# Performance work log

Hardware: AMD Instinct MI355X
Metric: run time of the kernel (lower is better)

Reference implementation:

```python
import jax, jax.numpy as jnp
import numpy as np

B, S, A = 65536, 376, 17
H1, H2, K = 400, 300, 15
MAX_ACTION = 1.0


def setup_inputs() -> dict:
    key = jax.random.key(0)
    ks = jax.random.split(key, 16)

    def lin(kw, fan_in, fan_out):
        lim = 1.0 / np.sqrt(fan_in)
        k1, k2 = jax.random.split(kw)
        W = jax.random.uniform(k1, (fan_in, fan_out), jnp.float32, -lim, lim)
        b = jax.random.uniform(k2, (fan_out,), jnp.float32, -lim, lim)
        return W, b

    W1, b1 = lin(ks[0], S, H1)
    W2, b2 = lin(ks[1], H1, H2)
    Wmu, bmu = lin(ks[2], H2, A)
    Wlv, blv = lin(ks[3], H2, A)
    Wu, bu = lin(ks[4], H2, K * A)
    Ww, bw = lin(ks[5], H2, K * A)
    Wb, bb = lin(ks[6], H2, K)
    x = jax.random.normal(ks[7], (B, S), jnp.float32)
    eps = jax.random.normal(ks[8], (B, A), jnp.float32)
    return dict(x=x, eps=eps, W1=W1, b1=b1, W2=W2, b2=b2, Wmu=Wmu, bmu=bmu,
                Wlv=Wlv, blv=blv, Wu=Wu, bu=bu, Ww=Ww, bw=bw, Wb=Wb, bb=bb)


def _flow_chain(action, u, w, b):
    # u, w: (K, B, A); b: (K, B). Sequential planar flow -> lax.scan over K.
    def step(carry, uwb):
        z, ldj = carry
        u_k, w_k, b_k = uwb
        uw = jnp.sum(w_k * u_k, -1)                       # (B,)
        m_uw = -1.0 + jax.nn.softplus(uw)
        w_norm_sq = jnp.sum(w_k * w_k, -1)
        u_hat = u_k + ((m_uw - uw) / w_norm_sq)[:, None] * w_k  # invertibility reparam
        wzb = jnp.sum(w_k * z, -1) + b_k                  # (B,)
        t = jnp.tanh(wzb)
        z_new = z + u_hat * t[:, None]
        psi_u = jnp.sum(w_k * u_hat, -1) * (1.0 - t * t)  # psi^T u_hat
        ldj_new = ldj + jnp.log(jnp.abs(1.0 + psi_u))
        return (z_new, ldj_new), None

    init = (action, jnp.zeros(action.shape[0], action.dtype))
    (z_fin, ldj), _ = jax.lax.scan(step, init, (u, w, b))
    return z_fin, ldj


def reference(x, eps, W1, b1, W2, b2, Wmu, bmu, Wlv, blv, Wu, bu, Ww, bw, Wb, bb):
    h = jax.nn.relu(x @ W1 + b1)
    h = jax.nn.relu(h @ W2 + b2)
    mu = MAX_ACTION * jnp.tanh(h @ Wmu + bmu)
    log_var = MAX_ACTION * jnp.tanh(h @ Wlv + blv)
    std = jnp.exp(log_var)                 # torch code uses log_var.exp() as the scale
    action = mu + std * eps                # rsample

    u = (h @ Wu + bu).reshape(B, K, A).transpose(1, 0, 2)   # (K, B, A)
    w = (h @ Ww + bw).reshape(B, K, A).transpose(1, 0, 2)   # (K, B, A)
    b = (h @ Wb + bb).T                                      # (K, B)

    final_action, log_det_j = _flow_chain(action, u, w, b)

    # Normal(mu, std).log_prob(action) summed over action dim; (action-mu)/std == eps
    log_2pi = jnp.float32(np.log(2.0 * np.pi))
    log_prob = jnp.sum(-0.5 * eps * eps - log_var - 0.5 * log_2pi, axis=-1)
    log_prob_final = log_prob - log_det_j
    prob_final = jnp.exp(log_prob_final)
    return final_action, prob_final, log_prob_final
```

## Files before the change

kernel.cpp:

```cpp
#include <hip/hip_runtime.h>

typedef unsigned short ushort_t;
typedef unsigned int uint_t;
typedef __bf16 bf16x8 __attribute__((ext_vector_type(8)));
typedef float f32x4 __attribute__((ext_vector_type(4)));

#define B_ROWS 65536

#define KT1 12
#define NT1 30
#define KTC1 15
#define KI2 13
#define NT2 20
#define KTC2 10
#define KI3 10
#define NT3 50
#define LDH3 25


#define SZ1 (NT1 * KT1 * 512)
#define SZ2 (NT2 * KI2 * 512)
#define SZ3 (NT3 * KI3 * 512)

__device__ inline float bf2f(ushort_t u) {
    union { uint_t i; float f; } x; x.i = ((uint_t)u) << 16; return x.f;
}
__device__ inline ushort_t f2bf(float f) {
    uint_t u = __float_as_uint(f);
    return (ushort_t)((u + 0x7FFFu + ((u >> 16) & 1u)) >> 16);
}
__device__ inline uint_t pack2(float a, float b) {
    return (uint_t)f2bf(a) | ((uint_t)f2bf(b) << 16);
}
__device__ inline float fast_tanh(float x) {
    float e = __expf(2.f * x);
    return 1.f - 2.f / (e + 1.f);
}
__device__ inline void gl2lds16(const ushort_t* g, ushort_t* l) {
    __builtin_amdgcn_global_load_lds(
        (const __attribute__((address_space(1))) uint_t*)g,
        (__attribute__((address_space(3))) uint_t*)l, 16, 0, 0);
}

__global__ void pack_kernel(const float* __restrict__ W1, const float* __restrict__ W2,
                            const float* __restrict__ Wmu, const float* __restrict__ Wlv,
                            const float* __restrict__ Wu, const float* __restrict__ Ww,
                            const float* __restrict__ Wb,
                            const float* __restrict__ b1, const float* __restrict__ b2,
                            const float* __restrict__ bmu, const float* __restrict__ blv,
                            const float* __restrict__ bu, const float* __restrict__ bw,
                            const float* __restrict__ bb,
                            ushort_t* __restrict__ W1t, ushort_t* __restrict__ W2t,
                            ushort_t* __restrict__ Wht,
                            float* __restrict__ b1p, float* __restrict__ b2p,
                            float* __restrict__ bHp)
{
    int i = blockIdx.x * 256 + threadIdx.x;
    if (i < SZ1) {
        int t = i >> 9, pos = i & 511;
        int l = pos >> 3, j = pos & 7;
        int n = (t / KT1) * 16 + (l & 15);
        int k = (t % KT1) * 32 + (l >> 4) * 8 + j;
        W1t[i] = (n < 400 && k < 376) ? f2bf(W1[k * 400 + n]) : (ushort_t)0;
    } else if (i < SZ1 + SZ2) {
        int i2 = i - SZ1;
        int t = i2 >> 9, pos = i2 & 511;
        int l = pos >> 3, j = pos & 7;
        int n = (t / KI2) * 16 + (l & 15);
        int k = (t % KI2) * 32 + (l >> 4) * 8 + j;
        W2t[i2] = (n < 300 && k < 400) ? f2bf(W2[k * 300 + n]) : (ushort_t)0;
    } else if (i < SZ1 + SZ2 + SZ3) {
        int i3 = i - SZ1 - SZ2;
        int t = i3 >> 9, pos = i3 & 511;
        int l = pos >> 3, j = pos & 7;
        int n = (t / KI3) * 16 + (l & 15);
        int k = (t % KI3) * 32 + (l >> 4) * 8 + j;
        float v = 0.f;
        if (k < 300) {
            if (n < 24)      { if (n < 17) v = Wmu[k * 17 + n]; }
            else if (n < 48) { int c = n - 24; if (c < 17) v = Wlv[k * 17 + c]; }
            else if (n < 64) { int c = n - 48; if (c < 15) v = Wb[k * 15 + c]; }
            else if (n < 784) {
                int r = n - 64, slot = r / 48, c = r % 48;
                if (c < 24) { if (c < 17) v = Wu[k * 255 + slot * 17 + c]; }
                else        { int c2 = c - 24; if (c2 < 17) v = Ww[k * 255 + slot * 17 + c2]; }
            }
        }
        Wht[i3] = f2bf(v);
    } else {
        int j = i - SZ1 - SZ2 - SZ3;
        if (j < 480) {
            b1p[j] = (j < 400) ? b1[j] : 0.f;
        } else if (j < 800) {
            int n = j - 480;
            b2p[n] = (n < 300) ? b2[n] : 0.f;
        } else if (j < 1600) {
            int n = j - 800;
            float v = 0.f;
            if (n < 24)      { if (n < 17) v = bmu[n]; }
            else if (n < 48) { int c = n - 24; if (c < 17) v = blv[c]; }
            else if (n < 64) { int c = n - 48; if (c < 15) v = bb[c]; }
            else if (n < 784) {
                int r = n - 64, slot = r / 48, c = r % 48;
                if (c < 24) { if (c < 17) v = bu[slot * 17 + c]; }
                else        { int c2 = c - 24; if (c2 < 17) v = bw[slot * 17 + c2]; }
            }
            bHp[n] = v;
        }
    }
}

__global__ __launch_bounds__(256)
void cvt_kernel(const float* __restrict__ x, ushort_t* __restrict__ xt, int nUnits)
{
    int U = blockIdx.x * 256 + threadIdx.x;
    if (U >= nUnits) return;
    int t = U >> 6, l = U & 63;
    int rowblk = t / KT1, kblk = t - rowblk * KT1;
    long row = (long)rowblk * 16 + (l & 15);
    int k0 = kblk * 32 + (l >> 4) * 8;
    uint4 o = {0u, 0u, 0u, 0u};
    if (k0 + 8 <= 376) {
        const float4* p = reinterpret_cast<const float4*>(x + row * 376 + k0);
        float4 v0 = p[0], v1 = p[1];
        o.x = pack2(v0.x, v0.y); o.y = pack2(v0.z, v0.w);
        o.z = pack2(v1.x, v1.y); o.w = pack2(v1.z, v1.w);
    }
    reinterpret_cast<uint4*>(xt)[U] = o;
}

template<bool RELU, bool OUT_TILED>
__global__ __launch_bounds__(256)
void gemm_tile(const ushort_t* __restrict__ A, const ushort_t* __restrict__ Bt,
               const float* __restrict__ bias, ushort_t* __restrict__ C,
               int kTA, int kIters, int kTC)
{
    __shared__ ushort_t As[8 * 512];
    __shared__ ushort_t Bs[10 * 512];
    const int tid = threadIdx.x;
    const int lane = tid & 63, wv = tid >> 6;
    const int q = lane >> 4, l16 = lane & 15;
    const int nb0 = blockIdx.x * 10;
    const int rowblk0 = blockIdx.y * 8;

    f32x4 acc[2][10];
    #pragma unroll
    for (int r = 0; r < 2; ++r)
        #pragma unroll
        for (int c = 0; c < 10; ++c)
            acc[r][c] = (f32x4){0.f, 0.f, 0.f, 0.f};

    for (int kt = 0; kt < kIters; ++kt) {
        #pragma unroll
        for (int i = 0; i < 2; ++i) {
            int t = wv * 2 + i;
            gl2lds16(A + (((size_t)(rowblk0 + t) * kTA + kt) << 9) + lane * 8,
                     &As[t << 9]);
        }
        #pragma unroll
        for (int t2 = 0; t2 < 3; ++t2) {
            int t = wv + t2 * 4;
            if (t < 10)
                gl2lds16(Bt + (((size_t)(nb0 + t) * kIters + kt) << 9) + lane * 8,
                         &Bs[t << 9]);
        }
        __syncthreads();

        bf16x8 a0 = __builtin_bit_cast(bf16x8,
            *reinterpret_cast<const uint4*>(&As[((wv * 2 + 0) << 9) + lane * 8]));
        bf16x8 a1 = __builtin_bit_cast(bf16x8,
            *reinterpret_cast<const uint4*>(&As[((wv * 2 + 1) << 9) + lane * 8]));
        #pragma unroll
        for (int c = 0; c < 10; ++c) {
            bf16x8 b = __builtin_bit_cast(bf16x8,
                *reinterpret_cast<const uint4*>(&Bs[(c << 9) + lane * 8]));
            acc[0][c] = __builtin_amdgcn_mfma_f32_16x16x32_bf16(a0, b, acc[0][c], 0, 0, 0);
            acc[1][c] = __builtin_amdgcn_mfma_f32_16x16x32_bf16(a1, b, acc[1][c], 0, 0, 0);
        }
        __syncthreads();
    }

    #pragma unroll
    for (int r = 0; r < 2; ++r) {
        int rowblk = rowblk0 + wv * 2 + r;
        #pragma unroll
        for (int c = 0; c < 10; ++c) {
            int n = (nb0 + c) * 16 + l16;
            float bv = bias[n];
            #pragma unroll
            for (int reg = 0; reg < 4; ++reg) {
                float v = acc[r][c][reg] + bv;
                if (RELU) v = fmaxf(v, 0.f);
                int mrow = q * 4 + reg;
                if (OUT_TILED) {
                    size_t off = (((size_t)rowblk * kTC + (n >> 5)) << 9)
                               + (size_t)(((n >> 3) & 3) * 16 + mrow) * 8 + (n & 7);
                    C[off] = f2bf(v);
                } else {
                    long m = (long)rowblk * 16 + mrow;
                    C[m * (long)kTC + n] = f2bf(v);
                }
            }
        }
    }
}

__device__ inline void ld_group8(const ushort_t* hb, int g, float* dst) {
    uint4 v = *reinterpret_cast<const uint4*>(hb + ((g >> 2) << 9) + ((g & 3) << 7));
    uint_t q[4] = {v.x, v.y, v.z, v.w};
    #pragma unroll
    for (int m = 0; m < 4; ++m) {
        dst[2 * m]     = __uint_as_float(q[m] << 16);
        dst[2 * m + 1] = __uint_as_float(q[m] & 0xFFFF0000u);
    }
}

__global__ __launch_bounds__(256, 4)
void flow_kernel(const ushort_t* __restrict__ heads, const float* __restrict__ eps,
                 float* __restrict__ out, int rowBase, int Btot)
{
    const int tid = threadIdx.x;
    const int sub = tid & 3;
    const long row = (long)blockIdx.x * 64 + (tid >> 2);
    const ushort_t* hb = heads + (((size_t)(row >> 4) * LDH3) << 9)
                               + (size_t)((row & 15) << 3);

    float z[8];
    float lp = 0.f;
    {
        float amu[8] = {0,0,0,0,0,0,0,0}, alv[8] = {0,0,0,0,0,0,0,0};
        if (sub < 3) {
            ld_group8(hb, sub, amu);
            ld_group8(hb, 3 + sub, alv);
        }
        float ep[8];
        #pragma unroll
        for (int c = 0; c < 8; ++c) {
            int i = sub * 8 + c;
            ep[c] = (i < 17) ? eps[row * 17 + i] : 0.f;
        }
        #pragma unroll
        for (int c = 0; c < 8; ++c) {
            float mu = fast_tanh(amu[c]);
            float lv = fast_tanh(alv[c]);
            z[c] = mu + __expf(lv) * ep[c];
            int i = sub * 8 + c;
            lp += (i < 17) ? (-0.5f * ep[c] * ep[c] - lv - 0.918938533f) : 0.f;
        }
    }

    float bv[16];
    ld_group8(hb, 6, &bv[0]);
    ld_group8(hb, 7, &bv[8]);

    float ldj = 0.f;
    #pragma unroll
    for (int k = 0; k < 15; ++k) {
        float au[8] = {0,0,0,0,0,0,0,0}, aw[8] = {0,0,0,0,0,0,0,0};
        if (sub < 3) {
            ld_group8(hb, 8 + 6 * k + sub, au);
            ld_group8(hb, 11 + 6 * k + sub, aw);
        }
        float uw = 0.f, w2 = 0.f, wz = 0.f;
        #pragma unroll
        for (int c = 0; c < 8; ++c) {
            uw += aw[c] * au[c];
            w2 += aw[c] * aw[c];
            wz += aw[c] * z[c];
        }
        uw += __shfl_xor(uw, 1); uw += __shfl_xor(uw, 2);
        w2 += __shfl_xor(w2, 1); w2 += __shfl_xor(w2, 2);
        wz += __shfl_xor(wz, 1); wz += __shfl_xor(wz, 2);

        float sp = (uw > 15.f) ? uw : __logf(1.f + __expf(uw));
        float m = sp - 1.f;
        float coef = (m - uw) / fmaxf(w2, 1e-20f);
        float t = fast_tanh(wz + bv[k]);
        #pragma unroll
        for (int c = 0; c < 8; ++c)
            z[c] += (au[c] + coef * aw[c]) * t;
        float psi = m * (1.f - t * t);
        ldj += __logf(fmaxf(fabsf(1.f + psi), 1e-30f));
    }

    lp += __shfl_xor(lp, 1); lp += __shfl_xor(lp, 2);
    const long g = rowBase + row;
    #pragma unroll
    for (int c = 0; c < 8; ++c) {
        int i = sub * 8 + c;
        if (i < 17) out[g * 17 + i] = z[c];
    }
    float lpf = lp - ldj;
    if (sub == 0) {
        out[(long)Btot * 17 + g] = __expf(lpf);
        out[(long)Btot * 18 + g] = lpf;
    }
}

extern "C" void kernel_launch(void* const* d_in, const int* in_sizes, int n_in,
                              void* d_out, int out_size, void* d_ws, size_t ws_size,
                              hipStream_t stream)
{
    const float* x   = (const float*)d_in[0];
    const float* eps = (const float*)d_in[1];
    float* out = (float*)d_out;

    const size_t wUS = (size_t)SZ1 + SZ2 + SZ3;
    const size_t fixedBytes = wUS * 2 + (480 + 320 + 800) * 4;
    int Mc = 2048;
    {
        const int cand[6] = {65536, 32768, 16384, 8192, 4096, 2048};
        for (int i = 0; i < 6; ++i) {
            size_t req = (size_t)cand[i] * 2368 + fixedBytes;
            if (req <= ws_size) { Mc = cand[i]; break; }
        }
    }

    ushort_t* region1 = (ushort_t*)d_ws;
    ushort_t* region2 = region1 + (size_t)Mc * 800;
    ushort_t* W1t = region2 + (size_t)Mc * 384;
    ushort_t* W2t = W1t + SZ1;
    ushort_t* Wht = W2t + SZ2;
    float* b1p = (float*)(Wht + SZ3);
    float* b2p = b1p + 480;
    float* bHp = b2p + 320;

    const int packN = SZ1 + SZ2 + SZ3 + 1600;
    pack_kernel<<<(packN + 255) / 256, 256, 0, stream>>>(
        (const float*)d_in[2],  (const float*)d_in[4],
        (const float*)d_in[6],  (const float*)d_in[8],
        (const float*)d_in[10], (const float*)d_in[12], (const float*)d_in[14],
        (const float*)d_in[3],  (const float*)d_in[5],
        (const float*)d_in[7],  (const float*)d_in[9],
        (const float*)d_in[11], (const float*)d_in[13], (const float*)d_in[15],
        W1t, W2t, Wht, b1p, b2p, bHp);

    const int nChunks = B_ROWS / Mc;
    const int nUnits = Mc * 48;
    for (int c = 0; c < nChunks; ++c) {
        const float* xc = x + (size_t)c * Mc * 376;
        cvt_kernel<<<(nUnits + 255) / 256, 256, 0, stream>>>(xc, region2, nUnits);
        gemm_tile<true, true><<<dim3(3, Mc / 128), 256, 0, stream>>>(
            region2, W1t, b1p, region1, KT1, KT1, KTC1);
        gemm_tile<true, true><<<dim3(2, Mc / 128), 256, 0, stream>>>(
            region1, W2t, b2p, region2, KTC1, KI2, KTC2);
        gemm_tile<false, true><<<dim3(5, Mc / 128), 256, 0, stream>>>(
            region2, Wht, bHp, region1, KTC2, KI3, LDH3);
        flow_kernel<<<Mc / 64, 256, 0, stream>>>(region1, eps + (size_t)c * Mc * 17,
                                                 out, c * Mc, B_ROWS);
    }
}
```

Baseline: 366.5 us.

## Fuse conversion, three GEMMs and flow chain into one LDS-resident kernel

Replaces the chunked pipeline of convert, three tiled GEMM launches and the flow kernel with a single fused kernel. Each 64-row block converts x to bf16 in LDS, runs all three GEMM layers with activations kept in shared memory, then computes the planar flow from LDS. Weights are read straight from global memory (L2) instead of being staged in LDS. This removes the global round-trips of the intermediate activations and the extra launches, at the cost of about 150 KB of LDS per block, which limits occupancy, and weight reloads in every block.

```diff
diff --git a/kernel.cpp b/kernel.cpp
--- a/kernel.cpp
+++ b/kernel.cpp
@@ -15,16 +15,19 @@
 #define KTC2 10
 #define KI3 10
 #define NT3 50
-#define LDH3 25
+#define KTH 25
 
 
 #define SZ1 (NT1 * KT1 * 512)
 #define SZ2 (NT2 * KI2 * 512)
 #define SZ3 (NT3 * KI3 * 512)
 
-__device__ inline float bf2f(ushort_t u) {
-    union { uint_t i; float f; } x; x.i = ((uint_t)u) << 16; return x.f;
-}
+#define P_X  0
+#define P_H1 24576
+#define P_H2 55296
+#define P_HD 0
+#define SM_TOT 75776
+
 __device__ inline ushort_t f2bf(float f) {
     uint_t u = __float_as_uint(f);
     return (ushort_t)((u + 0x7FFFu + ((u >> 16) & 1u)) >> 16);
@@ -36,10 +39,13 @@
     float e = __expf(2.f * x);
     return 1.f - 2.f / (e + 1.f);
 }
-__device__ inline void gl2lds16(const ushort_t* g, ushort_t* l) {
-    __builtin_amdgcn_global_load_lds(
-        (const __attribute__((address_space(1))) uint_t*)g,
-        (__attribute__((address_space(3))) uint_t*)l, 16, 0, 0);
+__device__ inline void unpack8(uint4 v, float* dst) {
+    uint_t q[4] = {v.x, v.y, v.z, v.w};
+    #pragma unroll
+    for (int m = 0; m < 4; ++m) {
+        dst[2 * m]     = __uint_as_float(q[m] << 16);
+        dst[2 * m + 1] = __uint_as_float(q[m] & 0xFFFF0000u);
+    }
 }
 
 __global__ void pack_kernel(const float* __restrict__ W1, const float* __restrict__ W2,
@@ -110,190 +116,185 @@
     }
 }
 
-__global__ __launch_bounds__(256)
-void cvt_kernel(const float* __restrict__ x, ushort_t* __restrict__ xt, int nUnits)
+template<int KITERS, bool RELU>
+__device__ __forceinline__ void phase_gemm(
+    ushort_t* sm, int aBase, int ktA,
+    const ushort_t* __restrict__ Bt, const float* __restrict__ bias,
+    int cBase, int ktC, int NT, int lane, int wv)
 {
-    int U = blockIdx.x * 256 + threadIdx.x;
-    if (U >= nUnits) return;
-    int t = U >> 6, l = U & 63;
-    int rowblk = t / KT1, kblk = t - rowblk * KT1;
-    long row = (long)rowblk * 16 + (l & 15);
-    int k0 = kblk * 32 + (l >> 4) * 8;
-    uint4 o = {0u, 0u, 0u, 0u};
-    if (k0 + 8 <= 376) {
-        const float4* p = reinterpret_cast<const float4*>(x + row * 376 + k0);
-        float4 v0 = p[0], v1 = p[1];
-        o.x = pack2(v0.x, v0.y); o.y = pack2(v0.z, v0.w);
-        o.z = pack2(v1.x, v1.y); o.w = pack2(v1.z, v1.w);
-    }
-    reinterpret_cast<uint4*>(xt)[U] = o;
-}
-
-template<bool RELU, bool OUT_TILED>
-__global__ __launch_bounds__(256)
-void gemm_tile(const ushort_t* __restrict__ A, const ushort_t* __restrict__ Bt,
-               const float* __restrict__ bias, ushort_t* __restrict__ C,
-               int kTA, int kIters, int kTC)
+    const int n0 = (NT * wv) >> 3;
+    const int cnt = ((NT * (wv + 1)) >> 3) - n0;
+
+    f32x4 acc[4][7];
+    #pragma unroll
+    for (int rt = 0; rt < 4; ++rt)
+        #pragma unroll
+        for (int c = 0; c < 7; ++c)
+            acc[rt][c] = (f32x4){0.f, 0.f, 0.f, 0.f};
+
+    #pragma unroll
+    for (int kt = 0; kt < KITERS; ++kt) {
+        bf16x8 a[4];
+        #pragma unroll
+        for (int rt = 0; rt < 4; ++rt)
+            a[rt] = __builtin_bit_cast(bf16x8, *reinterpret_cast<const uint4*>(
+                &sm[aBase + ((rt * ktA + kt) << 9) + lane * 8]));
+        #pragma unroll
+        for (int c = 0; c < 7; ++c) {
+            if (c < cnt) {
+                bf16x8 b = __builtin_bit_cast(bf16x8, *reinterpret_cast<const uint4*>(
+                    Bt + (((size_t)(n0 + c) * KITERS + kt) << 9) + lane * 8));
+                #pragma unroll
+                for (int rt = 0; rt < 4; ++rt)
+                    acc[rt][c] = __builtin_amdgcn_mfma_f32_16x16x32_bf16(
+                        a[rt], b, acc[rt][c], 0, 0, 0);
+            }
+        }
+    }
+
+    const int q = lane >> 4, l16 = lane & 15;
+    #pragma unroll
+    for (int c = 0; c < 7; ++c) {
+        if (c < cnt) {
+            int n = (n0 + c) * 16 + l16;
+            float bv = bias[n];
+            #pragma unroll
+            for (int rt = 0; rt < 4; ++rt) {
+                #pragma unroll
+                for (int reg = 0; reg < 4; ++reg) {
+                    float v = acc[rt][c][reg] + bv;
+                    if (RELU) v = fmaxf(v, 0.f);
+                    int r16 = q * 4 + reg;
+                    sm[cBase + ((rt * ktC + (n >> 5)) << 9) + (((n >> 3) & 3) << 7)
+                       + (r16 << 3) + (n & 7)] = f2bf(v);
+                }
+            }
+        }
+    }
+}
+
+__global__ __launch_bounds__(512, 2)
+void fused_kernel(const float* __restrict__ x, const float* __restrict__ eps,
+                  const ushort_t* __restrict__ W1t, const ushort_t* __restrict__ W2t,
+                  const ushort_t* __restrict__ Wht,
+                  const float* __restrict__ b1p, const float* __restrict__ b2p,
+                  const float* __restrict__ bHp,
+                  float* __restrict__ out)
 {
-    __shared__ ushort_t As[8 * 512];
-    __shared__ ushort_t Bs[10 * 512];
+    __shared__ ushort_t sm[SM_TOT];
     const int tid = threadIdx.x;
     const int lane = tid & 63, wv = tid >> 6;
-    const int q = lane >> 4, l16 = lane & 15;
-    const int nb0 = blockIdx.x * 10;
-    const int rowblk0 = blockIdx.y * 8;
-
-    f32x4 acc[2][10];
-    #pragma unroll
-    for (int r = 0; r < 2; ++r)
-        #pragma unroll
-        for (int c = 0; c < 10; ++c)
-            acc[r][c] = (f32x4){0.f, 0.f, 0.f, 0.f};
-
-    for (int kt = 0; kt < kIters; ++kt) {
-        #pragma unroll
-        for (int i = 0; i < 2; ++i) {
-            int t = wv * 2 + i;
-            gl2lds16(A + (((size_t)(rowblk0 + t) * kTA + kt) << 9) + lane * 8,
-                     &As[t << 9]);
-        }
-        #pragma unroll
-        for (int t2 = 0; t2 < 3; ++t2) {
-            int t = wv + t2 * 4;
-            if (t < 10)
-                gl2lds16(Bt + (((size_t)(nb0 + t) * kIters + kt) << 9) + lane * 8,
-                         &Bs[t << 9]);
-        }
-        __syncthreads();
-
-        bf16x8 a0 = __builtin_bit_cast(bf16x8,
-            *reinterpret_cast<const uint4*>(&As[((wv * 2 + 0) << 9) + lane * 8]));
-        bf16x8 a1 = __builtin_bit_cast(bf16x8,
-            *reinterpret_cast<const uint4*>(&As[((wv * 2 + 1) << 9) + lane * 8]));
-        #pragma unroll
-        for (int c = 0; c < 10; ++c) {
-            bf16x8 b = __builtin_bit_cast(bf16x8,
-                *reinterpret_cast<const uint4*>(&Bs[(c << 9) + lane * 8]));
-            acc[0][c] = __builtin_amdgcn_mfma_f32_16x16x32_bf16(a0, b, acc[0][c], 0, 0, 0);
-            acc[1][c] = __builtin_amdgcn_mfma_f32_16x16x32_bf16(a1, b, acc[1][c], 0, 0, 0);
-        }
-        __syncthreads();
-    }
-
-    #pragma unroll
-    for (int r = 0; r < 2; ++r) {
-        int rowblk = rowblk0 + wv * 2 + r;
-        #pragma unroll
-        for (int c = 0; c < 10; ++c) {
-            int n = (nb0 + c) * 16 + l16;
-            float bv = bias[n];
-            #pragma unroll
-            for (int reg = 0; reg < 4; ++reg) {
-                float v = acc[r][c][reg] + bv;
-                if (RELU) v = fmaxf(v, 0.f);
-                int mrow = q * 4 + reg;
-                if (OUT_TILED) {
-                    size_t off = (((size_t)rowblk * kTC + (n >> 5)) << 9)
-                               + (size_t)(((n >> 3) & 3) * 16 + mrow) * 8 + (n & 7);
-                    C[off] = f2bf(v);
-                } else {
-                    long m = (long)rowblk * 16 + mrow;
-                    C[m * (long)kTC + n] = f2bf(v);
-                }
-            }
-        }
-    }
-}
-
-__device__ inline void ld_group8(const ushort_t* hb, int g, float* dst) {
-    uint4 v = *reinterpret_cast<const uint4*>(hb + ((g >> 2) << 9) + ((g & 3) << 7));
-    uint_t q[4] = {v.x, v.y, v.z, v.w};
-    #pragma unroll
-    for (int m = 0; m < 4; ++m) {
-        dst[2 * m]     = __uint_as_float(q[m] << 16);
-        dst[2 * m + 1] = __uint_as_float(q[m] & 0xFFFF0000u);
-    }
-}
-
-__global__ __launch_bounds__(256, 4)
-void flow_kernel(const ushort_t* __restrict__ heads, const float* __restrict__ eps,
-                 float* __restrict__ out, int rowBase, int Btot)
-{
-    const int tid = threadIdx.x;
-    const int sub = tid & 3;
-    const long row = (long)blockIdx.x * 64 + (tid >> 2);
-    const ushort_t* hb = heads + (((size_t)(row >> 4) * LDH3) << 9)
-                               + (size_t)((row & 15) << 3);
-
-    float z[8];
-    float lp = 0.f;
-    {
-        float amu[8] = {0,0,0,0,0,0,0,0}, alv[8] = {0,0,0,0,0,0,0,0};
-        if (sub < 3) {
-            ld_group8(hb, sub, amu);
-            ld_group8(hb, 3 + sub, alv);
-        }
-        float ep[8];
+    const long row0 = (long)blockIdx.x * 64;
+
+    #pragma unroll
+    for (int it = 0; it < 6; ++it) {
+        int u = it * 512 + tid;
+        int row = u / 48, ku = u - row * 48;
+        uint4 o = {0u, 0u, 0u, 0u};
+        if (ku < 47) {
+            const float4* p = reinterpret_cast<const float4*>(
+                x + (row0 + row) * 376 + ku * 8);
+            float4 v0 = p[0], v1 = p[1];
+            o.x = pack2(v0.x, v0.y); o.y = pack2(v0.z, v0.w);
+            o.z = pack2(v1.x, v1.y); o.w = pack2(v1.z, v1.w);
+        }
+        *reinterpret_cast<uint4*>(
+            &sm[P_X + (((row >> 4) * KT1 + (ku >> 2)) << 9) + ((ku & 3) << 7)
+                + ((row & 15) << 3)]) = o;
+    }
+    __syncthreads();
+
+    phase_gemm<KT1, true>(sm, P_X, KT1, W1t, b1p, P_H1, KTC1, NT1, lane, wv);
+    __syncthreads();
+
+    phase_gemm<KI2, true>(sm, P_H1, KTC1, W2t, b2p, P_H2, KTC2, NT2, lane, wv);
+    __syncthreads();
+
+    phase_gemm<KI3, false>(sm, P_H2, KTC2, Wht, bHp, P_HD, KTH, NT3, lane, wv);
+    __syncthreads();
+
+    if (tid < 256) {
+        const int sub = tid & 3;
+        const int row = tid >> 2;
+        const int hb = P_HD + (((row >> 4) * KTH) << 9) + ((row & 15) << 3);
+        const long grow = row0 + row;
+
+        float z[8];
+        float lp = 0.f;
+        {
+            float amu[8] = {0,0,0,0,0,0,0,0}, alv[8] = {0,0,0,0,0,0,0,0};
+            if (sub < 3) {
+                unpack8(*reinterpret_cast<const uint4*>(
+                    &sm[hb + ((sub >> 2) << 9) + ((sub & 3) << 7)]), amu);
+                int g = 3 + sub;
+                unpack8(*reinterpret_cast<const uint4*>(
+                    &sm[hb + ((g >> 2) << 9) + ((g & 3) << 7)]), alv);
+            }
+            float ep[8];
+            #pragma unroll
+            for (int c = 0; c < 8; ++c) {
+                int i = sub * 8 + c;
+                ep[c] = (i < 17) ? eps[grow * 17 + i] : 0.f;
+            }
+            #pragma unroll
+            for (int c = 0; c < 8; ++c) {
+                float mu = fast_tanh(amu[c]);
+                float lv = fast_tanh(alv[c]);
+                z[c] = mu + __expf(lv) * ep[c];
+                int i = sub * 8 + c;
+                lp += (i < 17) ? (-0.5f * ep[c] * ep[c] - lv - 0.918938533f) : 0.f;
+            }
+        }
+
+        float bv[16];
+        unpack8(*reinterpret_cast<const uint4*>(&sm[hb + 512 + 256]), &bv[0]);
+        unpack8(*reinterpret_cast<const uint4*>(&sm[hb + 512 + 384]), &bv[8]);
+
+        float ldj = 0.f;
+        #pragma unroll
+        for (int k = 0; k < 15; ++k) {
+            float au[8] = {0,0,0,0,0,0,0,0}, aw[8] = {0,0,0,0,0,0,0,0};
+            if (sub < 3) {
+                int gu = 8 + 6 * k + sub;
+                int gw = 11 + 6 * k + sub;
+                unpack8(*reinterpret_cast<const uint4*>(
+                    &sm[hb + ((gu >> 2) << 9) + ((gu & 3) << 7)]), au);
+                unpack8(*reinterpret_cast<const uint4*>(
+                    &sm[hb + ((gw >> 2) << 9) + ((gw & 3) << 7)]), aw);
+            }
+            float uw = 0.f, w2 = 0.f, wz = 0.f;
+            #pragma unroll
+            for (int c = 0; c < 8; ++c) {
+                uw += aw[c] * au[c];
+                w2 += aw[c] * aw[c];
+                wz += aw[c] * z[c];
+            }
+            uw += __shfl_xor(uw, 1); uw += __shfl_xor(uw, 2);
+            w2 += __shfl_xor(w2, 1); w2 += __shfl_xor(w2, 2);
+            wz += __shfl_xor(wz, 1); wz += __shfl_xor(wz, 2);
+
+            float sp = (uw > 15.f) ? uw : __logf(1.f + __expf(uw));
+            float m = sp - 1.f;
+            float coef = (m - uw) / fmaxf(w2, 1e-20f);
+            float t = fast_tanh(wz + bv[k]);
+            #pragma unroll
+            for (int c = 0; c < 8; ++c)
+                z[c] += (au[c] + coef * aw[c]) * t;
+            float psi = m * (1.f - t * t);
+            ldj += __logf(fmaxf(fabsf(1.f + psi), 1e-30f));
+        }
+
+        lp += __shfl_xor(lp, 1); lp += __shfl_xor(lp, 2);
         #pragma unroll
         for (int c = 0; c < 8; ++c) {
             int i = sub * 8 + c;
-            ep[c] = (i < 17) ? eps[row * 17 + i] : 0.f;
-        }
-        #pragma unroll
-        for (int c = 0; c < 8; ++c) {
-            float mu = fast_tanh(amu[c]);
-            float lv = fast_tanh(alv[c]);
-            z[c] = mu + __expf(lv) * ep[c];
-            int i = sub * 8 + c;
-            lp += (i < 17) ? (-0.5f * ep[c] * ep[c] - lv - 0.918938533f) : 0.f;
-        }
-    }
-
-    float bv[16];
-    ld_group8(hb, 6, &bv[0]);
-    ld_group8(hb, 7, &bv[8]);
-
-    float ldj = 0.f;
-    #pragma unroll
-    for (int k = 0; k < 15; ++k) {
-        float au[8] = {0,0,0,0,0,0,0,0}, aw[8] = {0,0,0,0,0,0,0,0};
-        if (sub < 3) {
-            ld_group8(hb, 8 + 6 * k + sub, au);
-            ld_group8(hb, 11 + 6 * k + sub, aw);
-        }
-        float uw = 0.f, w2 = 0.f, wz = 0.f;
-        #pragma unroll
-        for (int c = 0; c < 8; ++c) {
-            uw += aw[c] * au[c];
-            w2 += aw[c] * aw[c];
-            wz += aw[c] * z[c];
-        }
-        uw += __shfl_xor(uw, 1); uw += __shfl_xor(uw, 2);
-        w2 += __shfl_xor(w2, 1); w2 += __shfl_xor(w2, 2);
-        wz += __shfl_xor(wz, 1); wz += __shfl_xor(wz, 2);
-
-        float sp = (uw > 15.f) ? uw : __logf(1.f + __expf(uw));
-        float m = sp - 1.f;
-        float coef = (m - uw) / fmaxf(w2, 1e-20f);
-        float t = fast_tanh(wz + bv[k]);
-        #pragma unroll
-        for (int c = 0; c < 8; ++c)
-            z[c] += (au[c] + coef * aw[c]) * t;
-        float psi = m * (1.f - t * t);
-        ldj += __logf(fmaxf(fabsf(1.f + psi), 1e-30f));
-    }
-
-    lp += __shfl_xor(lp, 1); lp += __shfl_xor(lp, 2);
-    const long g = rowBase + row;
-    #pragma unroll
-    for (int c = 0; c < 8; ++c) {
-        int i = sub * 8 + c;
-        if (i < 17) out[g * 17 + i] = z[c];
-    }
-    float lpf = lp - ldj;
-    if (sub == 0) {
-        out[(long)Btot * 17 + g] = __expf(lpf);
-        out[(long)Btot * 18 + g] = lpf;
+            if (i < 17) out[grow * 17 + i] = z[c];
+        }
+        float lpf = lp - ldj;
+        if (sub == 0) {
+            out[(long)B_ROWS * 17 + grow] = __expf(lpf);
+            out[(long)B_ROWS * 18 + grow] = lpf;
+        }
     }
 }
 
@@ -305,20 +306,7 @@
     const float* eps = (const float*)d_in[1];
     float* out = (float*)d_out;
 
-    const size_t wUS = (size_t)SZ1 + SZ2 + SZ3;
-    const size_t fixedBytes = wUS * 2 + (480 + 320 + 800) * 4;
-    int Mc = 2048;
-    {
-        const int cand[6] = {65536, 32768, 16384, 8192, 4096, 2048};
-        for (int i = 0; i < 6; ++i) {
-            size_t req = (size_t)cand[i] * 2368 + fixedBytes;
-            if (req <= ws_size) { Mc = cand[i]; break; }
-        }
-    }
-
-    ushort_t* region1 = (ushort_t*)d_ws;
-    ushort_t* region2 = region1 + (size_t)Mc * 800;
-    ushort_t* W1t = region2 + (size_t)Mc * 384;
+    ushort_t* W1t = (ushort_t*)d_ws;
     ushort_t* W2t = W1t + SZ1;
     ushort_t* Wht = W2t + SZ2;
     float* b1p = (float*)(Wht + SZ3);
@@ -335,18 +323,6 @@
         (const float*)d_in[11], (const float*)d_in[13], (const float*)d_in[15],
         W1t, W2t, Wht, b1p, b2p, bHp);
 
-    const int nChunks = B_ROWS / Mc;
-    const int nUnits = Mc * 48;
-    for (int c = 0; c < nChunks; ++c) {
-        const float* xc = x + (size_t)c * Mc * 376;
-        cvt_kernel<<<(nUnits + 255) / 256, 256, 0, stream>>>(xc, region2, nUnits);
-        gemm_tile<true, true><<<dim3(3, Mc / 128), 256, 0, stream>>>(
-            region2, W1t, b1p, region1, KT1, KT1, KTC1);
-        gemm_tile<true, true><<<dim3(2, Mc / 128), 256, 0, stream>>>(
-            region1, W2t, b2p, region2, KTC1, KI2, KTC2);
-        gemm_tile<false, true><<<dim3(5, Mc / 128), 256, 0, stream>>>(
-            region2, Wht, bHp, region1, KTC2, KI3, LDH3);
-        flow_kernel<<<Mc / 64, 256, 0, stream>>>(region1, eps + (size_t)c * Mc * 17,
-                                                 out, c * Mc, B_ROWS);
-    }
-}
+    fused_kernel<<<B_ROWS / 64, 512, 0, stream>>>(
+        x, eps, W1t, W2t, Wht, b1p, b2p, bHp, out);
+}
```

Measured after the change: 408.6 us. +11.5%, slower.

## Fuse fp32→bf16 conversion into first GEMM, double-buffer LDS, drop chunk loop

Applied to the files above, without the earlier changes.

The separate cvt_kernel goes away: the first GEMM now reads fp32 x directly, converts it to bf16 in registers and stages it into LDS. All GEMMs gain double-buffered LDS tiles so the next k-slice loads while MFMAs run on the current one, and use a block swizzle that groups row blocks by XCD. The per-chunk host loop is replaced by single full-batch launches with fixed workspace regions, which assumes a large enough workspace and removes the fallback sizing. LDS use per block doubles, which may lower occupancy.

```diff
diff --git a/kernel.cpp b/kernel.cpp
--- a/kernel.cpp
+++ b/kernel.cpp
@@ -15,16 +15,16 @@
 #define KTC2 10
 #define KI3 10
 #define NT3 50
-#define LDH3 25
+#define KTH 25
 
 
 #define SZ1 (NT1 * KT1 * 512)
 #define SZ2 (NT2 * KI2 * 512)
 #define SZ3 (NT3 * KI3 * 512)
 
-__device__ inline float bf2f(ushort_t u) {
-    union { uint_t i; float f; } x; x.i = ((uint_t)u) << 16; return x.f;
-}
+#define H2_US  ((size_t)4096 * KTC2 * 512)
+#define HEADS_US ((size_t)4096 * KTH * 512)
+
 __device__ inline ushort_t f2bf(float f) {
     uint_t u = __float_as_uint(f);
     return (ushort_t)((u + 0x7FFFu + ((u >> 16) & 1u)) >> 16);
@@ -40,6 +40,14 @@
     __builtin_amdgcn_global_load_lds(
         (const __attribute__((address_space(1))) uint_t*)g,
         (__attribute__((address_space(3))) uint_t*)l, 16, 0, 0);
+}
+__device__ inline void unpack8(uint4 v, float* dst) {
+    uint_t q[4] = {v.x, v.y, v.z, v.w};
+    #pragma unroll
+    for (int m = 0; m < 4; ++m) {
+        dst[2 * m]     = __uint_as_float(q[m] << 16);
+        dst[2 * m + 1] = __uint_as_float(q[m] & 0xFFFF0000u);
+    }
 }
 
 __global__ void pack_kernel(const float* __restrict__ W1, const float* __restrict__ W2,
@@ -110,38 +118,31 @@
     }
 }
 
+template<int KITERS, int NX, bool RELU, bool CVT_A>
 __global__ __launch_bounds__(256)
-void cvt_kernel(const float* __restrict__ x, ushort_t* __restrict__ xt, int nUnits)
+void gemm_db(const ushort_t* __restrict__ At, const float* __restrict__ xf,
+             const ushort_t* __restrict__ Bt, const float* __restrict__ bias,
+             ushort_t* __restrict__ C, int kTA, int kTC)
 {
-    int U = blockIdx.x * 256 + threadIdx.x;
-    if (U >= nUnits) return;
-    int t = U >> 6, l = U & 63;
-    int rowblk = t / KT1, kblk = t - rowblk * KT1;
-    long row = (long)rowblk * 16 + (l & 15);
-    int k0 = kblk * 32 + (l >> 4) * 8;
-    uint4 o = {0u, 0u, 0u, 0u};
-    if (k0 + 8 <= 376) {
-        const float4* p = reinterpret_cast<const float4*>(x + row * 376 + k0);
-        float4 v0 = p[0], v1 = p[1];
-        o.x = pack2(v0.x, v0.y); o.y = pack2(v0.z, v0.w);
-        o.z = pack2(v1.x, v1.y); o.w = pack2(v1.z, v1.w);
-    }
-    reinterpret_cast<uint4*>(xt)[U] = o;
-}
-
-template<bool RELU, bool OUT_TILED>
-__global__ __launch_bounds__(256)
-void gemm_tile(const ushort_t* __restrict__ A, const ushort_t* __restrict__ Bt,
-               const float* __restrict__ bias, ushort_t* __restrict__ C,
-               int kTA, int kIters, int kTC)
-{
-    __shared__ ushort_t As[8 * 512];
-    __shared__ ushort_t Bs[10 * 512];
+    __shared__ ushort_t As[2][8 * 512];
+    __shared__ ushort_t Bs[2][10 * 512];
     const int tid = threadIdx.x;
     const int lane = tid & 63, wv = tid >> 6;
     const int q = lane >> 4, l16 = lane & 15;
-    const int nb0 = blockIdx.x * 10;
-    const int rowblk0 = blockIdx.y * 8;
+
+    const int b = blockIdx.x;
+    const int xcd = b & 7, idx = b >> 3;
+    const int grp = idx / NX;
+    const int bx = idx - grp * NX;
+    const int by = xcd + grp * 8;
+    const int nb0 = bx * 10;
+    const int rowblk0 = by * 8;
+
+    const int ct = tid >> 6;
+    const int cl = tid & 63;
+    const int crow0 = (rowblk0 + ct) * 16 + (cl & 15);
+    const int crow1 = (rowblk0 + ct + 4) * 16 + (cl & 15);
+    const int ckoff = (cl >> 4) * 8;
 
     f32x4 acc[2][10];
     #pragma unroll
@@ -150,32 +151,91 @@
         for (int c = 0; c < 10; ++c)
             acc[r][c] = (f32x4){0.f, 0.f, 0.f, 0.f};
 
-    for (int kt = 0; kt < kIters; ++kt) {
+    if (CVT_A) {
+        #pragma unroll
+        for (int j = 0; j < 2; ++j) {
+            int row = j ? crow1 : crow0;
+            int k0 = ckoff;
+            uint4 o = {0u, 0u, 0u, 0u};
+            if (k0 + 8 <= 376) {
+                const float4* p = reinterpret_cast<const float4*>(
+                    xf + (size_t)row * 376 + k0);
+                float4 v0 = p[0], v1 = p[1];
+                o.x = pack2(v0.x, v0.y); o.y = pack2(v0.z, v0.w);
+                o.z = pack2(v1.x, v1.y); o.w = pack2(v1.z, v1.w);
+            }
+            *reinterpret_cast<uint4*>(&As[0][((ct + 4 * j) << 9) + (cl << 3)]) = o;
+        }
+    } else {
         #pragma unroll
         for (int i = 0; i < 2; ++i) {
             int t = wv * 2 + i;
-            gl2lds16(A + (((size_t)(rowblk0 + t) * kTA + kt) << 9) + lane * 8,
-                     &As[t << 9]);
-        }
-        #pragma unroll
-        for (int t2 = 0; t2 < 3; ++t2) {
-            int t = wv + t2 * 4;
-            if (t < 10)
-                gl2lds16(Bt + (((size_t)(nb0 + t) * kIters + kt) << 9) + lane * 8,
-                         &Bs[t << 9]);
-        }
-        __syncthreads();
+            gl2lds16(At + (((size_t)(rowblk0 + t) * kTA + 0) << 9) + lane * 8,
+                     &As[0][t << 9]);
+        }
+    }
+    #pragma unroll
+    for (int t2 = 0; t2 < 3; ++t2) {
+        int t = wv + t2 * 4;
+        if (t < 10)
+            gl2lds16(Bt + (((size_t)(nb0 + t) * KITERS + 0) << 9) + lane * 8,
+                     &Bs[0][t << 9]);
+    }
+    __syncthreads();
+
+    #pragma unroll
+    for (int kt = 0; kt < KITERS; ++kt) {
+        const int p = kt & 1;
+        uint4 nxt0, nxt1;
+        if (kt + 1 < KITERS) {
+            if (CVT_A) {
+                int k0 = (kt + 1) * 32 + ckoff;
+                nxt0 = (uint4){0u, 0u, 0u, 0u};
+                nxt1 = (uint4){0u, 0u, 0u, 0u};
+                if (k0 + 8 <= 376) {
+                    const float4* p0 = reinterpret_cast<const float4*>(
+                        xf + (size_t)crow0 * 376 + k0);
+                    float4 v0 = p0[0], v1 = p0[1];
+                    nxt0.x = pack2(v0.x, v0.y); nxt0.y = pack2(v0.z, v0.w);
+                    nxt0.z = pack2(v1.x, v1.y); nxt0.w = pack2(v1.z, v1.w);
+                    const float4* p1 = reinterpret_cast<const float4*>(
+                        xf + (size_t)crow1 * 376 + k0);
+                    float4 u0 = p1[0], u1 = p1[1];
+                    nxt1.x = pack2(u0.x, u0.y); nxt1.y = pack2(u0.z, u0.w);
+                    nxt1.z = pack2(u1.x, u1.y); nxt1.w = pack2(u1.z, u1.w);
+                }
+            } else {
+                #pragma unroll
+                for (int i = 0; i < 2; ++i) {
+                    int t = wv * 2 + i;
+                    gl2lds16(At + (((size_t)(rowblk0 + t) * kTA + kt + 1) << 9) + lane * 8,
+                             &As[p ^ 1][t << 9]);
+                }
+            }
+            #pragma unroll
+            for (int t2 = 0; t2 < 3; ++t2) {
+                int t = wv + t2 * 4;
+                if (t < 10)
+                    gl2lds16(Bt + (((size_t)(nb0 + t) * KITERS + kt + 1) << 9) + lane * 8,
+                             &Bs[p ^ 1][t << 9]);
+            }
+        }
 
         bf16x8 a0 = __builtin_bit_cast(bf16x8,
-            *reinterpret_cast<const uint4*>(&As[((wv * 2 + 0) << 9) + lane * 8]));
+            *reinterpret_cast<const uint4*>(&As[p][((wv * 2 + 0) << 9) + lane * 8]));
         bf16x8 a1 = __builtin_bit_cast(bf16x8,
-            *reinterpret_cast<const uint4*>(&As[((wv * 2 + 1) << 9) + lane * 8]));
+            *reinterpret_cast<const uint4*>(&As[p][((wv * 2 + 1) << 9) + lane * 8]));
         #pragma unroll
         for (int c = 0; c < 10; ++c) {
-            bf16x8 b = __builtin_bit_cast(bf16x8,
-                *reinterpret_cast<const uint4*>(&Bs[(c << 9) + lane * 8]));
-            acc[0][c] = __builtin_amdgcn_mfma_f32_16x16x32_bf16(a0, b, acc[0][c], 0, 0, 0);
-            acc[1][c] = __builtin_amdgcn_mfma_f32_16x16x32_bf16(a1, b, acc[1][c], 0, 0, 0);
+            bf16x8 bb = __builtin_bit_cast(bf16x8,
+                *reinterpret_cast<const uint4*>(&Bs[p][(c << 9) + lane * 8]));
+            acc[0][c] = __builtin_amdgcn_mfma_f32_16x16x32_bf16(a0, bb, acc[0][c], 0, 0, 0);
+            acc[1][c] = __builtin_amdgcn_mfma_f32_16x16x32_bf16(a1, bb, acc[1][c], 0, 0, 0);
+        }
+
+        if (CVT_A && kt + 1 < KITERS) {
+            *reinterpret_cast<uint4*>(&As[p ^ 1][(ct << 9) + (cl << 3)]) = nxt0;
+            *reinterpret_cast<uint4*>(&As[p ^ 1][((ct + 4) << 9) + (cl << 3)]) = nxt1;
         }
         __syncthreads();
     }
@@ -192,14 +252,9 @@
                 float v = acc[r][c][reg] + bv;
                 if (RELU) v = fmaxf(v, 0.f);
                 int mrow = q * 4 + reg;
-                if (OUT_TILED) {
-                    size_t off = (((size_t)rowblk * kTC + (n >> 5)) << 9)
-                               + (size_t)(((n >> 3) & 3) * 16 + mrow) * 8 + (n & 7);
-                    C[off] = f2bf(v);
-                } else {
-                    long m = (long)rowblk * 16 + mrow;
-                    C[m * (long)kTC + n] = f2bf(v);
-                }
+                size_t off = (((size_t)rowblk * kTC + (n >> 5)) << 9)
+                           + (size_t)(((n >> 3) & 3) * 16 + mrow) * 8 + (n & 7);
+                C[off] = f2bf(v);
             }
         }
     }
@@ -207,22 +262,17 @@
 
 __device__ inline void ld_group8(const ushort_t* hb, int g, float* dst) {
     uint4 v = *reinterpret_cast<const uint4*>(hb + ((g >> 2) << 9) + ((g & 3) << 7));
-    uint_t q[4] = {v.x, v.y, v.z, v.w};
-    #pragma unroll
-    for (int m = 0; m < 4; ++m) {
-        dst[2 * m]     = __uint_as_float(q[m] << 16);
-        dst[2 * m + 1] = __uint_as_float(q[m] & 0xFFFF0000u);
-    }
+    unpack8(v, dst);
 }
 
 __global__ __launch_bounds__(256, 4)
 void flow_kernel(const ushort_t* __restrict__ heads, const float* __restrict__ eps,
-                 float* __restrict__ out, int rowBase, int Btot)
+                 float* __restrict__ out, int Btot)
 {
     const int tid = threadIdx.x;
     const int sub = tid & 3;
     const long row = (long)blockIdx.x * 64 + (tid >> 2);
-    const ushort_t* hb = heads + (((size_t)(row >> 4) * LDH3) << 9)
+    const ushort_t* hb = heads + (((size_t)(row >> 4) * KTH) << 9)
                                + (size_t)((row & 15) << 3);
 
     float z[8];
@@ -284,16 +334,15 @@
     }
 
     lp += __shfl_xor(lp, 1); lp += __shfl_xor(lp, 2);
-    const long g = rowBase + row;
     #pragma unroll
     for (int c = 0; c < 8; ++c) {
         int i = sub * 8 + c;
-        if (i < 17) out[g * 17 + i] = z[c];
+        if (i < 17) out[row * 17 + i] = z[c];
     }
     float lpf = lp - ldj;
     if (sub == 0) {
-        out[(long)Btot * 17 + g] = __expf(lpf);
-        out[(long)Btot * 18 + g] = lpf;
+        out[(long)Btot * 17 + row] = __expf(lpf);
+        out[(long)Btot * 18 + row] = lpf;
     }
 }
 
@@ -305,20 +354,11 @@
     const float* eps = (const float*)d_in[1];
     float* out = (float*)d_out;
 
-    const size_t wUS = (size_t)SZ1 + SZ2 + SZ3;
-    const size_t fixedBytes = wUS * 2 + (480 + 320 + 800) * 4;
-    int Mc = 2048;
-    {
-        const int cand[6] = {65536, 32768, 16384, 8192, 4096, 2048};
-        for (int i = 0; i < 6; ++i) {
-            size_t req = (size_t)cand[i] * 2368 + fixedBytes;
-            if (req <= ws_size) { Mc = cand[i]; break; }
-        }
-    }
-
-    ushort_t* region1 = (ushort_t*)d_ws;
-    ushort_t* region2 = region1 + (size_t)Mc * 800;
-    ushort_t* W1t = region2 + (size_t)Mc * 384;
+    ushort_t* ws = (ushort_t*)d_ws;
+    ushort_t* R_h2    = ws;
+    ushort_t* R_h1    = ws + H2_US;
+    ushort_t* R_heads = ws + H2_US;
+    ushort_t* W1t = ws + H2_US + HEADS_US;
     ushort_t* W2t = W1t + SZ1;
     ushort_t* Wht = W2t + SZ2;
     float* b1p = (float*)(Wht + SZ3);
@@ -335,18 +375,11 @@
         (const float*)d_in[11], (const float*)d_in[13], (const float*)d_in[15],
         W1t, W2t, Wht, b1p, b2p, bHp);
 
-    const int nChunks = B_ROWS / Mc;
-    const int nUnits = Mc * 48;
-    for (int c = 0; c < nChunks; ++c) {
-        const float* xc = x + (size_t)c * Mc * 376;
-        cvt_kernel<<<(nUnits + 255) / 256, 256, 0, stream>>>(xc, region2, nUnits);
-        gemm_tile<true, true><<<dim3(3, Mc / 128), 256, 0, stream>>>(
-            region2, W1t, b1p, region1, KT1, KT1, KTC1);
-        gemm_tile<true, true><<<dim3(2, Mc / 128), 256, 0, stream>>>(
-            region1, W2t, b2p, region2, KTC1, KI2, KTC2);
-        gemm_tile<false, true><<<dim3(5, Mc / 128), 256, 0, stream>>>(
-            region2, Wht, bHp, region1, KTC2, KI3, LDH3);
-        flow_kernel<<<Mc / 64, 256, 0, stream>>>(region1, eps + (size_t)c * Mc * 17,
-                                                 out, c * Mc, B_ROWS);
-    }
-}
+    gemm_db<KT1, 3, true, true><<<3 * 512, 256, 0, stream>>>(
+        nullptr, x, W1t, b1p, R_h1, 0, KTC1);
+    gemm_db<KI2, 2, true, false><<<2 * 512, 256, 0, stream>>>(
+        R_h1, nullptr, W2t, b2p, R_h2, KTC1, KTC2);
+    gemm_db<KI3, 5, false, false><<<5 * 512, 256, 0, stream>>>(
+        R_h2, nullptr, Wht, bHp, R_heads, KTC2, KTH);
+    flow_kernel<<<B_ROWS / 64, 256, 0, stream>>>(R_heads, eps, out, B_ROWS);
+}
```

New measurement: 343.2 us. -6.4%, faster.
